# Optimization experiments

Measured on AMD Instinct MI355X. Metric: run time of the kernel, lower is better.

Reference implementation:

```python
import jax, jax.numpy as jnp
import numpy as np

NEG = -100000.0  # matches torch masked_fill constant

def setup_inputs() -> dict:
    key = jax.random.key(0)
    k1, k2, k3, k4 = jax.random.split(key, 4)
    B, T, D, H, S = 8, 2048, 1024, 8, 128
    features = jax.random.normal(k1, (B, T, D), dtype=jnp.float32)
    begins = jax.random.randint(k2, (B, S), 0, 2016, dtype=jnp.int64)
    widths = jax.random.randint(k3, (B, S), 1, 33, dtype=jnp.int64)
    ends = jnp.minimum(begins + widths, T)
    key_w = jax.random.normal(k4, (H, D), dtype=jnp.float32) / np.sqrt(D)
    key_b = jnp.zeros((H,), dtype=jnp.float32)
    return {"features": features, "begins": begins, "ends": ends,
            "key_w": key_w, "key_b": key_b}


def reference(features, begins, ends, key_w, key_b):
    # features: [B, T, D]; begins/ends: [B, S]
    B, T, D = features.shape
    H = key_w.shape[0]
    S = begins.shape[1]
    pos = jnp.arange(T)  # [T]
    # span mask [B, S, T]
    mask = (begins[..., None] <= pos) & (pos < ends[..., None])
    # key projection: [B, T, H]
    logits = jnp.einsum('btd,hd->bth', features, key_w) + key_b
    # masked softmax over T per (batch, span, head): [B, S, T, H]
    masked = jnp.where(mask[..., None], logits[:, None, :, :], NEG)
    weights = jax.nn.softmax(masked, axis=-2)
    # values = features reshaped to heads: [B, T, H, D//H]
    values = features.reshape(B, T, H, D // H)
    res = jnp.einsum('bthd,bsth->bshd', values, weights)  # [B, S, H, D//H]
    return res.reshape(B, S, D)
```

## Files before the change

### kernel.cpp

```cpp
#include <hip/hip_runtime.h>

#define B_  8
#define T_  2048
#define D_  1024
#define H_  8
#define S_  128
#define NSPAN (B_ * S_)
#define NBLK  256


__global__ void init_counter(unsigned int* __restrict__ c) { *c = 0u; }

__global__ __launch_bounds__(1024, 1) void span_pool_v6(
    const float* __restrict__ feat,
    const int* __restrict__ begins,
    const int* __restrict__ ends,
    const float* __restrict__ kw,
    const float* __restrict__ kb,
    float* __restrict__ out,
    unsigned int* __restrict__ counter)
{
    const int tid  = threadIdx.x;
    const int wv   = tid >> 6;
    const int lane = tid & 63;
    const int w    = wv >> 1;
    const int p    = wv & 1;
    const int coff = p * 512 + lane * 4;

    __shared__ __align__(16) float rowbuf[32 * D_];
    __shared__ __align__(16) float wts[32 * H_];
    __shared__ unsigned int s_slot[2];

    float4 kwr[4][4];
#pragma unroll
    for (int h = 0; h < 4; ++h)
#pragma unroll
        for (int c = 0; c < 4; ++c)
            kwr[h][c] = *(const float4*)(kw + (size_t)(4*p + h) * D_ + c * 256 + lane * 4);

    const float kbq = kb[4*p + (lane & 3)];

    auto dot_slot = [&](int r, float4 ra, float4 rb) {
        const float* rbo = &rowbuf[r * D_ + (p ? 0 : 512) + lane * 4];
        float4 fo0 = *(const float4*)(rbo);
        float4 fo1 = *(const float4*)(rbo + 256);
        const float4 f0 = p ? fo0 : ra;
        const float4 f1 = p ? fo1 : rb;
        const float4 f2 = p ? ra  : fo0;
        const float4 f3 = p ? rb  : fo1;
        float acc[4];
#pragma unroll
        for (int h = 0; h < 4; ++h) {
            acc[h] = f0.x*kwr[h][0].x + f0.y*kwr[h][0].y + f0.z*kwr[h][0].z + f0.w*kwr[h][0].w
                   + f1.x*kwr[h][1].x + f1.y*kwr[h][1].y + f1.z*kwr[h][1].z + f1.w*kwr[h][1].w
                   + f2.x*kwr[h][2].x + f2.y*kwr[h][2].y + f2.z*kwr[h][2].z + f2.w*kwr[h][2].w
                   + f3.x*kwr[h][3].x + f3.y*kwr[h][3].y + f3.z*kwr[h][3].z + f3.w*kwr[h][3].w;
        }
        const bool hb = lane & 1;
        float mine  = hb ? acc[1] : acc[0];
        float other = hb ? acc[0] : acc[1];
        float t0 = mine + __shfl_xor(other, 1, 64);
        mine  = hb ? acc[3] : acc[2];
        other = hb ? acc[2] : acc[3];
        float t1 = mine + __shfl_xor(other, 1, 64);
        const bool hb2 = (lane >> 1) & 1;
        mine  = hb2 ? t1 : t0;
        other = hb2 ? t0 : t1;
        float r0 = mine + __shfl_xor(other, 2, 64);
        r0 += __shfl_xor(r0,  4, 64);
        r0 += __shfl_xor(r0,  8, 64);
        r0 += __shfl_xor(r0, 16, 64);
        r0 += __shfl_xor(r0, 32, 64);
        if (lane < 4) wts[r * H_ + 4*p + lane] = r0 + kbq;
    };

    if (tid == 0) s_slot[0] = atomicAdd(counter, 1u);
    __syncthreads();
    int s = (int)s_slot[0];
    bool have = (s < NSPAN);
    int width = 0; size_t row0 = 0;
    float4 pfa0, pfa1, pfb0, pfb1;
    if (have) {
        const int bg = begins[s];
        width = ends[s] - bg;
        row0  = (size_t)(s >> 7) * T_ + bg;
        if (w < width) {
            const float* fr = feat + (row0 + w) * D_ + coff;
            pfa0 = *(const float4*)(fr); pfa1 = *(const float4*)(fr + 256);
        }
        if (w + 8 < width) {
            const float* fr = feat + (row0 + w + 8) * D_ + coff;
            pfb0 = *(const float4*)(fr); pfb1 = *(const float4*)(fr + 256);
        }
    }

    int it = 0;
    while (have) {
        if (tid == 0) s_slot[(it + 1) & 1] = atomicAdd(counter, 1u);

        float4 g2a, g2b, g3a, g3b;
        const bool v2 = (w + 16) < width, v3 = (w + 24) < width;
        if (v2) { const float* fr = feat + (row0 + w + 16) * D_ + coff;
                  g2a = *(const float4*)(fr); g2b = *(const float4*)(fr + 256); }
        if (v3) { const float* fr = feat + (row0 + w + 24) * D_ + coff;
                  g3a = *(const float4*)(fr); g3b = *(const float4*)(fr + 256); }
        if (w < width) {
            float* rb = &rowbuf[w * D_ + coff];
            *(float4*)(rb) = pfa0; *(float4*)(rb + 256) = pfa1;
        }
        if (w + 8 < width) {
            float* rb = &rowbuf[(w + 8) * D_ + coff];
            *(float4*)(rb) = pfb0; *(float4*)(rb + 256) = pfb1;
        }
        if (v2) { float* rb = &rowbuf[(w + 16) * D_ + coff];
                  *(float4*)(rb) = g2a; *(float4*)(rb + 256) = g2b; }
        if (v3) { float* rb = &rowbuf[(w + 24) * D_ + coff];
                  *(float4*)(rb) = g3a; *(float4*)(rb + 256) = g3b; }
        __syncthreads();

        if (w < width)      dot_slot(w,      pfa0, pfa1);
        if (w + 8 < width)  dot_slot(w + 8,  pfb0, pfb1);
        if (v2)             dot_slot(w + 16, g2a, g2b);
        if (v3)             dot_slot(w + 24, g3a, g3b);
        __syncthreads();

        const int snext = (int)s_slot[(it + 1) & 1];
        const bool havenext = (snext < NSPAN);
        int width_n = 0; size_t row0_n = 0;
        if (havenext) {
            const int bg = begins[snext];
            width_n = ends[snext] - bg;
            row0_n  = (size_t)(snext >> 7) * T_ + bg;
            if (w < width_n) {
                const float* fr = feat + (row0_n + w) * D_ + coff;
                pfa0 = *(const float4*)(fr); pfa1 = *(const float4*)(fr + 256);
            }
            if (w + 8 < width_n) {
                const float* fr = feat + (row0_n + w + 8) * D_ + coff;
                pfb0 = *(const float4*)(fr); pfb1 = *(const float4*)(fr + 256);
            }
        }

        if (tid < 64) {
            float4 lv = *(const float4*)&wts[lane * 4];
            const int w8 = width * H_;
            float v0 = (4 * lane + 0 < w8) ? lv.x : -1e30f;
            float v1 = (4 * lane + 1 < w8) ? lv.y : -1e30f;
            float v2s = (4 * lane + 2 < w8) ? lv.z : -1e30f;
            float v3s = (4 * lane + 3 < w8) ? lv.w : -1e30f;

            float m0 = v0, m1 = v1, m2 = v2s, m3 = v3s;
#pragma unroll
            for (int off = 2; off <= 32; off <<= 1) {
                m0 = fmaxf(m0, __shfl_xor(m0, off, 64));
                m1 = fmaxf(m1, __shfl_xor(m1, off, 64));
                m2 = fmaxf(m2, __shfl_xor(m2, off, 64));
                m3 = fmaxf(m3, __shfl_xor(m3, off, 64));
            }
            float e0 = __expf(v0 - m0);
            float e1 = __expf(v1 - m1);
            float e2 = __expf(v2s - m2);
            float e3 = __expf(v3s - m3);
            float s0 = e0, s1 = e1, s2 = e2, s3 = e3;
#pragma unroll
            for (int off = 2; off <= 32; off <<= 1) {
                s0 += __shfl_xor(s0, off, 64);
                s1 += __shfl_xor(s1, off, 64);
                s2 += __shfl_xor(s2, off, 64);
                s3 += __shfl_xor(s3, off, 64);
            }
            *(float4*)&wts[lane * 4] =
                make_float4(e0 / s0, e1 / s1, e2 / s2, e3 / s3);
        }
        __syncthreads();

        if (tid < 256) {
            const int ha = tid >> 5;
            float4 a = make_float4(0.f, 0.f, 0.f, 0.f);
#pragma unroll 4
            for (int k = 0; k < width; ++k) {
                const float4 rv = *(const float4*)&rowbuf[k * D_ + tid * 4];
                const float wt = wts[k * H_ + ha];
                a.x += wt * rv.x; a.y += wt * rv.y;
                a.z += wt * rv.z; a.w += wt * rv.w;
            }
            *(float4*)(out + (size_t)s * D_ + tid * 4) = a;
        }
        __syncthreads();

        s = snext; have = havenext; width = width_n; row0 = row0_n; ++it;
    }
}

extern "C" void kernel_launch(void* const* d_in, const int* in_sizes, int n_in,
                              void* d_out, int out_size, void* d_ws, size_t ws_size,
                              hipStream_t stream) {
    const float* feat   = (const float*)d_in[0];
    const int*   begins = (const int*)d_in[1];
    const int*   ends   = (const int*)d_in[2];
    const float* kw     = (const float*)d_in[3];
    const float* kb     = (const float*)d_in[4];
    float*       out    = (float*)d_out;
    unsigned int* counter = (unsigned int*)d_ws;

    init_counter<<<1, 1, 0, stream>>>(counter);
    span_pool_v6<<<NBLK, 1024, 0, stream>>>(feat, begins, ends, kw, kb, out, counter);
}
```

Baseline: 131.7 us.

## Repartition span rows into 4 column-quarter groups with paired-row logit dots

```diff
diff --git a/kernel.cpp b/kernel.cpp
--- a/kernel.cpp
+++ b/kernel.cpp
@@ -11,7 +11,11 @@
 
 __global__ void init_counter(unsigned int* __restrict__ c) { *c = 0u; }
 
-__global__ __launch_bounds__(1024, 1) void span_pool_v6(
+__device__ __forceinline__ float dot4(float4 a, float4 b) {
+    return a.x*b.x + a.y*b.y + a.z*b.z + a.w*b.w;
+}
+
+__global__ __launch_bounds__(1024) void span_pool_v7(
     const float* __restrict__ feat,
     const int* __restrict__ begins,
     const int* __restrict__ ends,
@@ -23,55 +27,55 @@
     const int tid  = threadIdx.x;
     const int wv   = tid >> 6;
     const int lane = tid & 63;
-    const int w    = wv >> 1;
-    const int p    = wv & 1;
-    const int coff = p * 512 + lane * 4;
+    const int g    = wv >> 2;
+    const int p    = wv & 3;
+    const int coff = p * 256 + lane * 4;
 
     __shared__ __align__(16) float rowbuf[32 * D_];
     __shared__ __align__(16) float wts[32 * H_];
     __shared__ unsigned int s_slot[2];
 
-    float4 kwr[4][4];
-#pragma unroll
-    for (int h = 0; h < 4; ++h)
+    float4 kwr[2][4];
+#pragma unroll
+    for (int h = 0; h < 2; ++h)
 #pragma unroll
         for (int c = 0; c < 4; ++c)
-            kwr[h][c] = *(const float4*)(kw + (size_t)(4*p + h) * D_ + c * 256 + lane * 4);
-
-    const float kbq = kb[4*p + (lane & 3)];
-
-    auto dot_slot = [&](int r, float4 ra, float4 rb) {
-        const float* rbo = &rowbuf[r * D_ + (p ? 0 : 512) + lane * 4];
-        float4 fo0 = *(const float4*)(rbo);
-        float4 fo1 = *(const float4*)(rbo + 256);
-        const float4 f0 = p ? fo0 : ra;
-        const float4 f1 = p ? fo1 : rb;
-        const float4 f2 = p ? ra  : fo0;
-        const float4 f3 = p ? rb  : fo1;
-        float acc[4];
-#pragma unroll
-        for (int h = 0; h < 4; ++h) {
-            acc[h] = f0.x*kwr[h][0].x + f0.y*kwr[h][0].y + f0.z*kwr[h][0].z + f0.w*kwr[h][0].w
-                   + f1.x*kwr[h][1].x + f1.y*kwr[h][1].y + f1.z*kwr[h][1].z + f1.w*kwr[h][1].w
-                   + f2.x*kwr[h][2].x + f2.y*kwr[h][2].y + f2.z*kwr[h][2].z + f2.w*kwr[h][2].w
-                   + f3.x*kwr[h][3].x + f3.y*kwr[h][3].y + f3.z*kwr[h][3].z + f3.w*kwr[h][3].w;
-        }
-        const bool hb = lane & 1;
-        float mine  = hb ? acc[1] : acc[0];
-        float other = hb ? acc[0] : acc[1];
-        float t0 = mine + __shfl_xor(other, 1, 64);
-        mine  = hb ? acc[3] : acc[2];
-        other = hb ? acc[2] : acc[3];
-        float t1 = mine + __shfl_xor(other, 1, 64);
-        const bool hb2 = (lane >> 1) & 1;
-        mine  = hb2 ? t1 : t0;
-        other = hb2 ? t0 : t1;
-        float r0 = mine + __shfl_xor(other, 2, 64);
-        r0 += __shfl_xor(r0,  4, 64);
-        r0 += __shfl_xor(r0,  8, 64);
-        r0 += __shfl_xor(r0, 16, 64);
-        r0 += __shfl_xor(r0, 32, 64);
-        if (lane < 4) wts[r * H_ + 4*p + lane] = r0 + kbq;
+            kwr[h][c] = *(const float4*)(kw + (size_t)(2*p + h) * D_ + c * 256 + lane * 4);
+
+    const float kbq = kb[2*p + (lane & 1)];
+
+    auto dot_pair = [&](int rA, int width) {
+        const int rB = rA + 4;
+        float aA0 = 0.f, aA1 = 0.f, aB0 = 0.f, aB1 = 0.f;
+#pragma unroll
+        for (int c = 0; c < 4; ++c) {
+            const float4 fa = *(const float4*)&rowbuf[rA * D_ + c * 256 + lane * 4];
+            aA0 += dot4(fa, kwr[0][c]);
+            aA1 += dot4(fa, kwr[1][c]);
+        }
+#pragma unroll
+        for (int c = 0; c < 4; ++c) {
+            const float4 fb = *(const float4*)&rowbuf[rB * D_ + c * 256 + lane * 4];
+            aB0 += dot4(fb, kwr[0][c]);
+            aB1 += dot4(fb, kwr[1][c]);
+        }
+        const bool h0 = lane & 1;
+        float mA = h0 ? aA1 : aA0, oA = h0 ? aA0 : aA1;
+        float tA = mA + __shfl_xor(oA, 1, 64);
+        float mB = h0 ? aB1 : aB0, oB = h0 ? aB0 : aB1;
+        float tB = mB + __shfl_xor(oB, 1, 64);
+        const bool h1 = (lane >> 1) & 1;
+        float mT = h1 ? tB : tA, oT = h1 ? tA : tB;
+        float t = mT + __shfl_xor(oT, 2, 64);
+        t += __shfl_xor(t,  4, 64);
+        t += __shfl_xor(t,  8, 64);
+        t += __shfl_xor(t, 16, 64);
+        t += __shfl_xor(t, 32, 64);
+        if (lane < 4) {
+            const int rw = rA + 4 * (lane >> 1);
+            if (rw < width)
+                wts[rw * H_ + 2*p + (lane & 1)] = t + kbq;
+        }
     };
 
     if (tid == 0) s_slot[0] = atomicAdd(counter, 1u);
@@ -79,49 +83,47 @@
     int s = (int)s_slot[0];
     bool have = (s < NSPAN);
     int width = 0; size_t row0 = 0;
-    float4 pfa0, pfa1, pfb0, pfb1;
+    float4 pf0, pf1;
     if (have) {
         const int bg = begins[s];
         width = ends[s] - bg;
         row0  = (size_t)(s >> 7) * T_ + bg;
-        if (w < width) {
-            const float* fr = feat + (row0 + w) * D_ + coff;
-            pfa0 = *(const float4*)(fr); pfa1 = *(const float4*)(fr + 256);
-        }
-        if (w + 8 < width) {
-            const float* fr = feat + (row0 + w + 8) * D_ + coff;
-            pfb0 = *(const float4*)(fr); pfb1 = *(const float4*)(fr + 256);
-        }
+        if (g < width)     pf0 = *(const float4*)(feat + (row0 + g)     * D_ + coff);
+        if (g + 4 < width) pf1 = *(const float4*)(feat + (row0 + g + 4) * D_ + coff);
     }
 
     int it = 0;
     while (have) {
         if (tid == 0) s_slot[(it + 1) & 1] = atomicAdd(counter, 1u);
 
-        float4 g2a, g2b, g3a, g3b;
-        const bool v2 = (w + 16) < width, v3 = (w + 24) < width;
-        if (v2) { const float* fr = feat + (row0 + w + 16) * D_ + coff;
-                  g2a = *(const float4*)(fr); g2b = *(const float4*)(fr + 256); }
-        if (v3) { const float* fr = feat + (row0 + w + 24) * D_ + coff;
-                  g3a = *(const float4*)(fr); g3b = *(const float4*)(fr + 256); }
-        if (w < width) {
-            float* rb = &rowbuf[w * D_ + coff];
-            *(float4*)(rb) = pfa0; *(float4*)(rb + 256) = pfa1;
-        }
-        if (w + 8 < width) {
-            float* rb = &rowbuf[(w + 8) * D_ + coff];
-            *(float4*)(rb) = pfb0; *(float4*)(rb + 256) = pfb1;
-        }
-        if (v2) { float* rb = &rowbuf[(w + 16) * D_ + coff];
-                  *(float4*)(rb) = g2a; *(float4*)(rb + 256) = g2b; }
-        if (v3) { float* rb = &rowbuf[(w + 24) * D_ + coff];
-                  *(float4*)(rb) = g3a; *(float4*)(rb + 256) = g3b; }
-        __syncthreads();
-
-        if (w < width)      dot_slot(w,      pfa0, pfa1);
-        if (w + 8 < width)  dot_slot(w + 8,  pfb0, pfb1);
-        if (v2)             dot_slot(w + 16, g2a, g2b);
-        if (v3)             dot_slot(w + 24, g3a, g3b);
+        if (g < width)     { *(float4*)&rowbuf[(g)     * D_ + coff] = pf0; }
+        if (g + 4 < width) { *(float4*)&rowbuf[(g + 4) * D_ + coff] = pf1; }
+        {
+            float4 t0, t1, t2;
+            const bool b0 = g +  8 < width, b1 = g + 12 < width, b2 = g + 16 < width;
+            if (b0) t0 = *(const float4*)(feat + (row0 + g +  8) * D_ + coff);
+            if (b1) t1 = *(const float4*)(feat + (row0 + g + 12) * D_ + coff);
+            if (b2) t2 = *(const float4*)(feat + (row0 + g + 16) * D_ + coff);
+            if (b0) *(float4*)&rowbuf[(g +  8) * D_ + coff] = t0;
+            if (b1) *(float4*)&rowbuf[(g + 12) * D_ + coff] = t1;
+            if (b2) *(float4*)&rowbuf[(g + 16) * D_ + coff] = t2;
+        }
+        {
+            float4 t0, t1, t2;
+            const bool b0 = g + 20 < width, b1 = g + 24 < width, b2 = g + 28 < width;
+            if (b0) t0 = *(const float4*)(feat + (row0 + g + 20) * D_ + coff);
+            if (b1) t1 = *(const float4*)(feat + (row0 + g + 24) * D_ + coff);
+            if (b2) t2 = *(const float4*)(feat + (row0 + g + 28) * D_ + coff);
+            if (b0) *(float4*)&rowbuf[(g + 20) * D_ + coff] = t0;
+            if (b1) *(float4*)&rowbuf[(g + 24) * D_ + coff] = t1;
+            if (b2) *(float4*)&rowbuf[(g + 28) * D_ + coff] = t2;
+        }
+        __syncthreads();
+
+        if (g < width)      dot_pair(g,      width);
+        if (g +  8 < width) dot_pair(g +  8, width);
+        if (g + 16 < width) dot_pair(g + 16, width);
+        if (g + 24 < width) dot_pair(g + 24, width);
         __syncthreads();
 
         const int snext = (int)s_slot[(it + 1) & 1];
@@ -131,14 +133,8 @@
             const int bg = begins[snext];
             width_n = ends[snext] - bg;
             row0_n  = (size_t)(snext >> 7) * T_ + bg;
-            if (w < width_n) {
-                const float* fr = feat + (row0_n + w) * D_ + coff;
-                pfa0 = *(const float4*)(fr); pfa1 = *(const float4*)(fr + 256);
-            }
-            if (w + 8 < width_n) {
-                const float* fr = feat + (row0_n + w + 8) * D_ + coff;
-                pfb0 = *(const float4*)(fr); pfb1 = *(const float4*)(fr + 256);
-            }
+            if (g < width_n)     pf0 = *(const float4*)(feat + (row0_n + g)     * D_ + coff);
+            if (g + 4 < width_n) pf1 = *(const float4*)(feat + (row0_n + g + 4) * D_ + coff);
         }
 
         if (tid < 64) {
@@ -146,10 +142,10 @@
             const int w8 = width * H_;
             float v0 = (4 * lane + 0 < w8) ? lv.x : -1e30f;
             float v1 = (4 * lane + 1 < w8) ? lv.y : -1e30f;
-            float v2s = (4 * lane + 2 < w8) ? lv.z : -1e30f;
-            float v3s = (4 * lane + 3 < w8) ? lv.w : -1e30f;
-
-            float m0 = v0, m1 = v1, m2 = v2s, m3 = v3s;
+            float v2 = (4 * lane + 2 < w8) ? lv.z : -1e30f;
+            float v3 = (4 * lane + 3 < w8) ? lv.w : -1e30f;
+
+            float m0 = v0, m1 = v1, m2 = v2, m3 = v3;
 #pragma unroll
             for (int off = 2; off <= 32; off <<= 1) {
                 m0 = fmaxf(m0, __shfl_xor(m0, off, 64));
@@ -159,8 +155,8 @@
             }
             float e0 = __expf(v0 - m0);
             float e1 = __expf(v1 - m1);
-            float e2 = __expf(v2s - m2);
-            float e3 = __expf(v3s - m3);
+            float e2 = __expf(v2 - m2);
+            float e3 = __expf(v3 - m3);
             float s0 = e0, s1 = e1, s2 = e2, s3 = e3;
 #pragma unroll
             for (int off = 2; off <= 32; off <<= 1) {
@@ -204,5 +200,5 @@
     unsigned int* counter = (unsigned int*)d_ws;
 
     init_counter<<<1, 1, 0, stream>>>(counter);
-    span_pool_v6<<<NBLK, 1024, 0, stream>>>(feat, begins, ends, kw, kb, out, counter);
+    span_pool_v7<<<NBLK, 1024, 0, stream>>>(feat, begins, ends, kw, kb, out, counter);
 }
```

Measured after the change: 121.0 us. 8.1% less time.
